# Kernel tuning notes

Hardware: AMD Instinct MI355X
Metric: run time of the kernel (lower is better)

## Reference

```python
import jax, jax.numpy as jnp
import numpy as np

N = 100000      # nodes (H3 lattice cells)
E = 600000      # directed edges (avg degree ~6, hexagonal)
D_IN, D_H, D_E = 256, 128, 64


def _init_linear(key, fan_in, fan_out):
    kw, kb = jax.random.split(key)
    s = 1.0 / np.sqrt(fan_in)
    W = jax.random.uniform(kw, (fan_in, fan_out), jnp.float32, -s, s)
    b = jax.random.uniform(kb, (fan_out,), jnp.float32, -s, s)
    return W, b


def setup_inputs() -> dict:
    key = jax.random.key(0)
    ks = jax.random.split(key, 8)
    W1, b1 = _init_linear(ks[2], D_IN, D_H)
    W2, b2 = _init_linear(ks[3], D_H, D_H)
    W3, b3 = _init_linear(ks[4], D_H, D_E)
    Wd1, bd1 = _init_linear(ks[5], D_E, D_H)
    Wd2, bd2 = _init_linear(ks[6], D_H, D_IN)
    return {
        "x": jax.random.normal(ks[0], (N, D_IN), jnp.float32),
        "edge_index": jax.random.randint(ks[1], (2, E), 0, N, dtype=jnp.int64),
        "W1": W1, "b1": b1, "W2": W2, "b2": b2, "W3": W3, "b3": b3,
        "Wd1": Wd1, "bd1": bd1, "Wd2": Wd2, "bd2": bd2,
    }


def _gcn_conv(x, src, dst, W, b):
    """PyG GCNConv: add self-loops, sym deg^{-1/2} norm, linear, scatter-add, bias."""
    n = x.shape[0]
    h = x @ W                                                  # [N, out]
    ones = jnp.ones(src.shape[0], x.dtype)
    deg = jax.ops.segment_sum(ones, dst, num_segments=n) + 1.0  # +1 for self-loop
    dinv = jax.lax.rsqrt(deg)                                   # deg >= 1 always
    coef = dinv[src] * dinv[dst]                                # [E]
    agg = jax.ops.segment_sum(h[src] * coef[:, None], dst, num_segments=n)
    agg = agg + h * (dinv * dinv)[:, None]                      # self-loop term
    return agg + b


def reference(x, edge_index, W1, b1, W2, b2, W3, b3, Wd1, bd1, Wd2, bd2):
    src, dst = edge_index[0], edge_index[1]
    # Encoder (dropout is identity in eval mode)
    h = jax.nn.relu(_gcn_conv(x, src, dst, W1, b1))
    h = jax.nn.relu(_gcn_conv(h, src, dst, W2, b2))
    z = _gcn_conv(h, src, dst, W3, b3)                          # [N, D_E]
    # Decoder
    x_hat = jax.nn.relu(z @ Wd1 + bd1) @ Wd2 + bd2              # [N, D_IN]
    return (z, x_hat)
```

## Files before the change

kernel.cpp:

```cpp
#include <hip/hip_runtime.h>

#define DIN 256
#define DH  128
#define DE  64

typedef __attribute__((ext_vector_type(8))) short short8;
typedef __attribute__((ext_vector_type(4))) float f32x4;
typedef __attribute__((ext_vector_type(4))) unsigned short us4;

__device__ inline unsigned short f2bf(float f) {
    unsigned u = __float_as_uint(f);
    return (unsigned short)((u + 0x7FFFu + ((u >> 16) & 1u)) >> 16);
}
__device__ inline float bf2f(unsigned short h) {
    return __uint_as_float((unsigned)h << 16);
}

__device__ inline void gload16(const void* g, void* l) {
    __builtin_amdgcn_global_load_lds(
        (const __attribute__((address_space(1))) void*)g,
        (__attribute__((address_space(3))) void*)l, 16, 0, 0);
}


__global__ void init_counts_kernel(int* __restrict__ counts, int n) {
    int i = blockIdx.x * blockDim.x + threadIdx.x;
    if (i < n) counts[i] = 0;
}

__global__ void count_edges_kernel(const int* __restrict__ dst,
                                   int* __restrict__ counts, int E) {
    int e = blockIdx.x * blockDim.x + threadIdx.x;
    if (e < E) atomicAdd(&counts[dst[e]], 1);
}

__global__ void dinv_kernel(const int* __restrict__ counts,
                            float* __restrict__ dinv, int n) {
    int i = blockIdx.x * blockDim.x + threadIdx.x;
    if (i < n) dinv[i] = rsqrtf((float)counts[i] + 1.0f);
}

__global__ void scan1_kernel(const int* __restrict__ counts,
                             int* __restrict__ rowptr,
                             int* __restrict__ blocksums, int n) {
    __shared__ int sd[256];
    int t = threadIdx.x;
    int base = blockIdx.x * 1024 + t * 4;
    int v[4];
#pragma unroll
    for (int i = 0; i < 4; i++) v[i] = (base + i < n) ? counts[base + i] : 0;
    int tsum = v[0] + v[1] + v[2] + v[3];
    sd[t] = tsum;
    __syncthreads();
    for (int off = 1; off < 256; off <<= 1) {
        int x = (t >= off) ? sd[t - off] : 0;
        __syncthreads();
        sd[t] += x;
        __syncthreads();
    }
    int p = sd[t] - tsum;
#pragma unroll
    for (int i = 0; i < 4; i++) {
        if (base + i < n) rowptr[base + i] = p;
        p += v[i];
    }
    if (t == 255) blocksums[blockIdx.x] = sd[255];
}

__global__ void scan2_kernel(int* __restrict__ blocksums, int nb) {
    if (threadIdx.x == 0 && blockIdx.x == 0) {
        int run = 0;
        for (int i = 0; i < nb; i++) {
            int x = blocksums[i];
            blocksums[i] = run;
            run += x;
        }
    }
}

__global__ void scan3_kernel(int* __restrict__ rowptr, int* __restrict__ cursor,
                             const int* __restrict__ blocksums, int n, int E) {
    int i = blockIdx.x * blockDim.x + threadIdx.x;
    if (i < n) {
        int r = rowptr[i] + blocksums[i >> 10];
        rowptr[i] = r;
        cursor[i] = r;
    }
    if (i == 0) rowptr[n] = E;
}

__global__ void fill_csr_kernel(const int* __restrict__ src,
                                const int* __restrict__ dst,
                                const float* __restrict__ dinv,
                                int* __restrict__ cursor,
                                int* __restrict__ csr_src,
                                float* __restrict__ csr_coef, int E) {
    int e = blockIdx.x * blockDim.x + threadIdx.x;
    if (e >= E) return;
    int s = src[e], d = dst[e];
    int pos = atomicAdd(&cursor[d], 1);
    csr_src[pos] = s;
    csr_coef[pos] = dinv[s] * dinv[d];
}


__global__ void wsplit_kernel(const float* __restrict__ W,
                              unsigned short* __restrict__ Wh,
                              unsigned short* __restrict__ Wl, int K, int N) {
    int i = blockIdx.x * blockDim.x + threadIdx.x;
    if (i >= K * N) return;
    int k = i / N, n = i % N;
    float v = W[i];
    unsigned short h = f2bf(v);
    Wh[(size_t)n * K + k] = h;
    Wl[(size_t)n * K + k] = f2bf(v - bf2f(h));
}


template <int K, int CF, bool AFP32, bool BIAS, bool RELU, bool SPLIT>
__global__ __launch_bounds__(256, 2) void mfma_gemm(
    const void* __restrict__ Agh, const void* __restrict__ Agl,
    const unsigned short* __restrict__ Wh,
    const unsigned short* __restrict__ Wl, const float* __restrict__ bias,
    float* __restrict__ C, unsigned short* __restrict__ Oh,
    unsigned short* __restrict__ Ol, int M, int NN) {
    __shared__ unsigned short Ath[128 * 64];
    __shared__ unsigned short Atl[128 * 64];

    int t = threadIdx.x;
    int wid = t >> 6;
    int l = t & 63;
    int lr = l & 15, lk = l >> 4;
    int row0 = blockIdx.x * 128;
    int col0 = blockIdx.y * (CF * 16);

    f32x4 acc0[CF], acc1[CF];
#pragma unroll
    for (int j = 0; j < CF; j++) {
        acc0[j] = (f32x4){0.f, 0.f, 0.f, 0.f};
        acc1[j] = (f32x4){0.f, 0.f, 0.f, 0.f};
    }

    for (int c = 0; c < K / 64; ++c) {
        int k0 = c * 64;
        if (AFP32) {
            const float* A = (const float*)Agh;
#pragma unroll
            for (int i = 0; i < 4; i++) {
                int row = i * 32 + (t >> 3);
                int gr = row0 + row;
                if (gr >= M) gr = M - 1;
                int ss = (t & 7) ^ (row & 7);
                const float* sp = A + (size_t)gr * K + k0 + ss * 8;
                float4 f0 = *(const float4*)sp;
                float4 f1 = *(const float4*)(sp + 4);
                float fv[8] = {f0.x, f0.y, f0.z, f0.w,
                               f1.x, f1.y, f1.z, f1.w};
                short8 hv, lv;
#pragma unroll
                for (int e = 0; e < 8; e++) {
                    unsigned short h = f2bf(fv[e]);
                    hv[e] = (short)h;
                    lv[e] = (short)f2bf(fv[e] - bf2f(h));
                }
                int li = (i * 256 + t) * 8;
                *(short8*)&Ath[li] = hv;
                *(short8*)&Atl[li] = lv;
            }
        } else {
            const unsigned short* Ah = (const unsigned short*)Agh;
            const unsigned short* Al = (const unsigned short*)Agl;
#pragma unroll
            for (int i = 0; i < 4; i++) {
                int row = i * 32 + (t >> 3);
                int gr = row0 + row;
                if (gr >= M) gr = M - 1;
                int ss = (t & 7) ^ (row & 7);
                size_t go = (size_t)gr * K + k0 + ss * 8;
                gload16(Ah + go, &Ath[(i * 256 + t) * 8]);
                gload16(Al + go, &Atl[(i * 256 + t) * 8]);
            }
        }
        __syncthreads();

#pragma unroll
        for (int ks = 0; ks < 2; ks++) {
            int r0 = wid * 32 + lr;
            int r1 = r0 + 16;
            int s = ks * 4 + lk;
            short8 a0h = *(const short8*)&Ath[r0 * 64 + (s ^ (r0 & 7)) * 8];
            short8 a0l = *(const short8*)&Atl[r0 * 64 + (s ^ (r0 & 7)) * 8];
            short8 a1h = *(const short8*)&Ath[r1 * 64 + (s ^ (r1 & 7)) * 8];
            short8 a1l = *(const short8*)&Atl[r1 * 64 + (s ^ (r1 & 7)) * 8];
            int kg = k0 + ks * 32 + lk * 8;
#pragma unroll
            for (int j = 0; j < CF; j++) {
                size_t wo = (size_t)(col0 + j * 16 + lr) * K + kg;
                short8 bh = *(const short8*)(Wh + wo);
                short8 bl = *(const short8*)(Wl + wo);
                acc0[j] = __builtin_amdgcn_mfma_f32_16x16x32_bf16(
                    a0h, bh, acc0[j], 0, 0, 0);
                acc0[j] = __builtin_amdgcn_mfma_f32_16x16x32_bf16(
                    a0l, bh, acc0[j], 0, 0, 0);
                acc0[j] = __builtin_amdgcn_mfma_f32_16x16x32_bf16(
                    a0h, bl, acc0[j], 0, 0, 0);
                acc1[j] = __builtin_amdgcn_mfma_f32_16x16x32_bf16(
                    a1h, bh, acc1[j], 0, 0, 0);
                acc1[j] = __builtin_amdgcn_mfma_f32_16x16x32_bf16(
                    a1l, bh, acc1[j], 0, 0, 0);
                acc1[j] = __builtin_amdgcn_mfma_f32_16x16x32_bf16(
                    a1h, bl, acc1[j], 0, 0, 0);
            }
        }
        __syncthreads();
    }

#pragma unroll
    for (int j = 0; j < CF; j++) {
        int col = col0 + j * 16 + lr;
        float bb = BIAS ? bias[col] : 0.f;
#pragma unroll
        for (int e = 0; e < 4; e++) {
            int r = row0 + wid * 32 + lk * 4 + e;
#pragma unroll
            for (int rf = 0; rf < 2; rf++) {
                int rr = r + rf * 16;
                if (rr >= M) continue;
                float v = (rf ? acc1[j][e] : acc0[j][e]) + bb;
                if (RELU) v = fmaxf(v, 0.f);
                if (SPLIT) {
                    unsigned short h = f2bf(v);
                    Oh[(size_t)rr * NN + col] = h;
                    Ol[(size_t)rr * NN + col] = f2bf(v - bf2f(h));
                } else {
                    C[(size_t)rr * NN + col] = v;
                }
            }
        }
    }
}


template <int D, bool RELU, bool WF32>
__global__ __launch_bounds__(256) void agg_kernel(
    const float* __restrict__ h, const float* __restrict__ dinv,
    const int* __restrict__ rowptr, const int* __restrict__ csr_src,
    const float* __restrict__ csr_coef, const float* __restrict__ bias,
    unsigned short* __restrict__ outh, unsigned short* __restrict__ outl,
    float* __restrict__ outf, int n) {
    constexpr int TPN = D / 16;
    constexpr int NPB = 256 / TPN;
    int v = blockIdx.x * NPB + threadIdx.x / TPN;
    int d = threadIdx.x % TPN;
    if (v >= n) return;

    float di = dinv[v];
    float s2 = di * di;
    const float* hv = h + (size_t)v * D + d * 4;
    float4 acc[4];
#pragma unroll
    for (int i = 0; i < 4; i++) {
        float4 sv = *(const float4*)(hv + i * TPN * 4);
        float4 bv = *(const float4*)&bias[(i * TPN + d) * 4];
        acc[i].x = fmaf(sv.x, s2, bv.x);
        acc[i].y = fmaf(sv.y, s2, bv.y);
        acc[i].z = fmaf(sv.z, s2, bv.z);
        acc[i].w = fmaf(sv.w, s2, bv.w);
    }

    int e0 = rowptr[v], e1 = rowptr[v + 1];
    int e = e0;
    for (; e + 2 <= e1; e += 2) {
        int s0 = csr_src[e], s1 = csr_src[e + 1];
        float c0 = csr_coef[e], c1 = csr_coef[e + 1];
        const float* p0 = h + (size_t)s0 * D + d * 4;
        const float* p1 = h + (size_t)s1 * D + d * 4;
        float4 g0[4], g1[4];
#pragma unroll
        for (int i = 0; i < 4; i++) g0[i] = *(const float4*)(p0 + i * TPN * 4);
#pragma unroll
        for (int i = 0; i < 4; i++) g1[i] = *(const float4*)(p1 + i * TPN * 4);
#pragma unroll
        for (int i = 0; i < 4; i++) {
            acc[i].x = fmaf(g0[i].x, c0, acc[i].x);
            acc[i].y = fmaf(g0[i].y, c0, acc[i].y);
            acc[i].z = fmaf(g0[i].z, c0, acc[i].z);
            acc[i].w = fmaf(g0[i].w, c0, acc[i].w);
            acc[i].x = fmaf(g1[i].x, c1, acc[i].x);
            acc[i].y = fmaf(g1[i].y, c1, acc[i].y);
            acc[i].z = fmaf(g1[i].z, c1, acc[i].z);
            acc[i].w = fmaf(g1[i].w, c1, acc[i].w);
        }
    }
    if (e < e1) {
        int s0 = csr_src[e];
        float c0 = csr_coef[e];
        const float* p0 = h + (size_t)s0 * D + d * 4;
#pragma unroll
        for (int i = 0; i < 4; i++) {
            float4 g = *(const float4*)(p0 + i * TPN * 4);
            acc[i].x = fmaf(g.x, c0, acc[i].x);
            acc[i].y = fmaf(g.y, c0, acc[i].y);
            acc[i].z = fmaf(g.z, c0, acc[i].z);
            acc[i].w = fmaf(g.w, c0, acc[i].w);
        }
    }

#pragma unroll
    for (int i = 0; i < 4; i++) {
        if (RELU) {
            acc[i].x = fmaxf(acc[i].x, 0.f);
            acc[i].y = fmaxf(acc[i].y, 0.f);
            acc[i].z = fmaxf(acc[i].z, 0.f);
            acc[i].w = fmaxf(acc[i].w, 0.f);
        }
        size_t o = (size_t)v * D + (i * TPN + d) * 4;
        float av[4] = {acc[i].x, acc[i].y, acc[i].z, acc[i].w};
        us4 hw, lw;
#pragma unroll
        for (int q = 0; q < 4; q++) {
            unsigned short hh = f2bf(av[q]);
            hw[q] = hh;
            lw[q] = f2bf(av[q] - bf2f(hh));
        }
        *(us4*)&outh[o] = hw;
        *(us4*)&outl[o] = lw;
        if (WF32) *(float4*)&outf[o] = acc[i];
    }
}


extern "C" void kernel_launch(void* const* d_in, const int* in_sizes, int n_in,
                              void* d_out, int out_size, void* d_ws,
                              size_t ws_size, hipStream_t stream) {
    const float* x   = (const float*)d_in[0];
    const int*   ei  = (const int*)d_in[1];
    const float* W1  = (const float*)d_in[2];
    const float* b1  = (const float*)d_in[3];
    const float* W2  = (const float*)d_in[4];
    const float* b2  = (const float*)d_in[5];
    const float* W3  = (const float*)d_in[6];
    const float* b3  = (const float*)d_in[7];
    const float* Wd1 = (const float*)d_in[8];
    const float* bd1 = (const float*)d_in[9];
    const float* Wd2 = (const float*)d_in[10];
    const float* bd2 = (const float*)d_in[11];

    const int N = in_sizes[0] / DIN;
    const int E = in_sizes[1] / 2;
    const int* src = ei;
    const int* dst = ei + E;

    char* w = (char*)d_ws;
    auto alloc = [&](size_t bytes) -> char* {
        char* p = w;
        w += (bytes + 255) & ~(size_t)255;
        return p;
    };
    int*   counts    = (int*)alloc((size_t)N * 4);
    float* dinv      = (float*)alloc((size_t)N * 4);
    int*   rowptr    = (int*)alloc((size_t)(N + 1) * 4);
    int*   cursor    = (int*)alloc((size_t)N * 4);
    int*   blocksums = (int*)alloc(4096);
    int*   csr_src   = (int*)alloc((size_t)E * 4);
    float* csr_coef  = (float*)alloc((size_t)E * 4);
    unsigned short* hh = (unsigned short*)alloc((size_t)N * DH * 2);
    unsigned short* hl = (unsigned short*)alloc((size_t)N * DH * 2);
    unsigned short* W1h  = (unsigned short*)alloc(DIN * DH * 2);
    unsigned short* W1l  = (unsigned short*)alloc(DIN * DH * 2);
    unsigned short* W2h  = (unsigned short*)alloc(DH * DH * 2);
    unsigned short* W2l  = (unsigned short*)alloc(DH * DH * 2);
    unsigned short* W3h  = (unsigned short*)alloc(DH * DE * 2);
    unsigned short* W3l  = (unsigned short*)alloc(DH * DE * 2);
    unsigned short* Wd1h = (unsigned short*)alloc(DE * DH * 2);
    unsigned short* Wd1l = (unsigned short*)alloc(DE * DH * 2);
    unsigned short* Wd2h = (unsigned short*)alloc(DH * DIN * 2);
    unsigned short* Wd2l = (unsigned short*)alloc(DH * DIN * 2);

    float* zout = (float*)d_out;
    float* xhat = zout + (size_t)N * DE;
    float* S1   = xhat;
    unsigned short* zh = (unsigned short*)(xhat + (size_t)N * DH);
    unsigned short* zl = zh + (size_t)N * DE;
    unsigned short* rh = hh;
    unsigned short* rl = hl;

    dim3 blk(256);
    int gN = (N + 255) / 256, gE = (E + 255) / 256;

    init_counts_kernel<<<gN, blk, 0, stream>>>(counts, N);
    count_edges_kernel<<<gE, blk, 0, stream>>>(dst, counts, E);
    dinv_kernel<<<gN, blk, 0, stream>>>(counts, dinv, N);
    int nb = (N + 1023) / 1024;
    scan1_kernel<<<nb, blk, 0, stream>>>(counts, rowptr, blocksums, N);
    scan2_kernel<<<1, 64, 0, stream>>>(blocksums, nb);
    scan3_kernel<<<gN, blk, 0, stream>>>(rowptr, cursor, blocksums, N, E);
    fill_csr_kernel<<<gE, blk, 0, stream>>>(src, dst, dinv, cursor, csr_src,
                                            csr_coef, E);

    wsplit_kernel<<<(DIN * DH + 255) / 256, blk, 0, stream>>>(W1, W1h, W1l,
                                                              DIN, DH);
    wsplit_kernel<<<(DH * DH + 255) / 256, blk, 0, stream>>>(W2, W2h, W2l,
                                                             DH, DH);
    wsplit_kernel<<<(DH * DE + 255) / 256, blk, 0, stream>>>(W3, W3h, W3l,
                                                             DH, DE);
    wsplit_kernel<<<(DE * DH + 255) / 256, blk, 0, stream>>>(Wd1, Wd1h, Wd1l,
                                                             DE, DH);
    wsplit_kernel<<<(DH * DIN + 255) / 256, blk, 0, stream>>>(Wd2, Wd2h, Wd2l,
                                                              DH, DIN);

    int gm = (N + 127) / 128;

    mfma_gemm<DIN, 8, true, false, false, false><<<dim3(gm, 1), blk, 0,
        stream>>>(x, nullptr, W1h, W1l, nullptr, S1, nullptr, nullptr, N, DH);
    agg_kernel<DH, true, false><<<(N + 31) / 32, blk, 0, stream>>>(
        S1, dinv, rowptr, csr_src, csr_coef, b1, hh, hl, nullptr, N);
    mfma_gemm<DH, 8, false, false, false, false><<<dim3(gm, 1), blk, 0,
        stream>>>(hh, hl, W2h, W2l, nullptr, S1, nullptr, nullptr, N, DH);
    agg_kernel<DH, true, false><<<(N + 31) / 32, blk, 0, stream>>>(
        S1, dinv, rowptr, csr_src, csr_coef, b2, hh, hl, nullptr, N);
    mfma_gemm<DH, 4, false, false, false, false><<<dim3(gm, 1), blk, 0,
        stream>>>(hh, hl, W3h, W3l, nullptr, S1, nullptr, nullptr, N, DE);
    agg_kernel<DE, false, true><<<(N + 63) / 64, blk, 0, stream>>>(
        S1, dinv, rowptr, csr_src, csr_coef, b3, zh, zl, zout, N);
    mfma_gemm<DE, 8, false, true, true, true><<<dim3(gm, 1), blk, 0,
        stream>>>(zh, zl, Wd1h, Wd1l, bd1, nullptr, rh, rl, N, DH);
    mfma_gemm<DH, 8, false, true, false, false><<<dim3(gm, 2), blk, 0,
        stream>>>(rh, rl, Wd2h, Wd2l, bd2, xhat, nullptr, nullptr, N, DIN);
}
```

Measured before the change: 736.8 us.

## Stage pre-tiled swizzled weight chunks in LDS for MFMA GEMMs

Weights are now split into bf16 hi/lo and written in a per-column-block, per-K-chunk tiled layout with an XOR swizzle. Each GEMM block copies its weight chunk into shared memory with async global-to-LDS loads alongside the A tile. The MFMA inner loop then reads B fragments from LDS instead of issuing global loads per fragment. This cuts repeated global/L2 traffic for weights, at the cost of extra LDS use, which may lower occupancy.

```diff
diff --git a/kernel.cpp b/kernel.cpp
--- a/kernel.cpp
+++ b/kernel.cpp
@@ -104,35 +104,46 @@
 }
 
 
-__global__ void wsplit_kernel(const float* __restrict__ W,
-                              unsigned short* __restrict__ Wh,
-                              unsigned short* __restrict__ Wl, int K, int N) {
+__global__ void wtile_kernel(const float* __restrict__ W,
+                             unsigned short* __restrict__ WtH,
+                             unsigned short* __restrict__ WtL, int K, int N,
+                             int CF16) {
     int i = blockIdx.x * blockDim.x + threadIdx.x;
     if (i >= K * N) return;
     int k = i / N, n = i % N;
     float v = W[i];
     unsigned short h = f2bf(v);
-    Wh[(size_t)n * K + k] = h;
-    Wl[(size_t)n * K + k] = f2bf(v - bf2f(h));
+    unsigned short lo = f2bf(v - bf2f(h));
+    int cb = n / CF16, cl = n % CF16;
+    int chunk = k >> 6, kk = k & 63;
+    int s = kk >> 3, e = kk & 7;
+    size_t idx = (size_t)(cb * (K >> 6) + chunk) * (CF16 * 64) + cl * 64 +
+                 ((s ^ (cl & 7)) * 8) + e;
+    WtH[idx] = h;
+    WtL[idx] = lo;
 }
 
 
 template <int K, int CF, bool AFP32, bool BIAS, bool RELU, bool SPLIT>
 __global__ __launch_bounds__(256, 2) void mfma_gemm(
     const void* __restrict__ Agh, const void* __restrict__ Agl,
-    const unsigned short* __restrict__ Wh,
-    const unsigned short* __restrict__ Wl, const float* __restrict__ bias,
+    const unsigned short* __restrict__ WtH,
+    const unsigned short* __restrict__ WtL, const float* __restrict__ bias,
     float* __restrict__ C, unsigned short* __restrict__ Oh,
     unsigned short* __restrict__ Ol, int M, int NN) {
+    constexpr int CF16 = CF * 16;
+    constexpr int CHUNKS = K / 64;
     __shared__ unsigned short Ath[128 * 64];
     __shared__ unsigned short Atl[128 * 64];
+    __shared__ unsigned short Bth[CF16 * 64];
+    __shared__ unsigned short Btl[CF16 * 64];
 
     int t = threadIdx.x;
     int wid = t >> 6;
     int l = t & 63;
     int lr = l & 15, lk = l >> 4;
     int row0 = blockIdx.x * 128;
-    int col0 = blockIdx.y * (CF * 16);
+    int col0 = blockIdx.y * CF16;
 
     f32x4 acc0[CF], acc1[CF];
 #pragma unroll
@@ -141,8 +152,15 @@
         acc1[j] = (f32x4){0.f, 0.f, 0.f, 0.f};
     }
 
-    for (int c = 0; c < K / 64; ++c) {
+    for (int c = 0; c < CHUNKS; ++c) {
         int k0 = c * 64;
+        size_t bbase = (size_t)(blockIdx.y * CHUNKS + c) * (CF16 * 64);
+#pragma unroll
+        for (int i = 0; i < CF16 / 32; i++) {
+            int idx = (i * 256 + t) * 8;
+            gload16(WtH + bbase + idx, &Bth[idx]);
+            gload16(WtL + bbase + idx, &Btl[idx]);
+        }
         if (AFP32) {
             const float* A = (const float*)Agh;
 #pragma unroll
@@ -192,12 +210,11 @@
             short8 a0l = *(const short8*)&Atl[r0 * 64 + (s ^ (r0 & 7)) * 8];
             short8 a1h = *(const short8*)&Ath[r1 * 64 + (s ^ (r1 & 7)) * 8];
             short8 a1l = *(const short8*)&Atl[r1 * 64 + (s ^ (r1 & 7)) * 8];
-            int kg = k0 + ks * 32 + lk * 8;
 #pragma unroll
             for (int j = 0; j < CF; j++) {
-                size_t wo = (size_t)(col0 + j * 16 + lr) * K + kg;
-                short8 bh = *(const short8*)(Wh + wo);
-                short8 bl = *(const short8*)(Wl + wo);
+                int bo = (j * 16 + lr) * 64 + ((s ^ (lr & 7)) * 8);
+                short8 bh = *(const short8*)&Bth[bo];
+                short8 bl = *(const short8*)&Btl[bo];
                 acc0[j] = __builtin_amdgcn_mfma_f32_16x16x32_bf16(
                     a0h, bh, acc0[j], 0, 0, 0);
                 acc0[j] = __builtin_amdgcn_mfma_f32_16x16x32_bf16(
@@ -398,16 +415,16 @@
     fill_csr_kernel<<<gE, blk, 0, stream>>>(src, dst, dinv, cursor, csr_src,
                                             csr_coef, E);
 
-    wsplit_kernel<<<(DIN * DH + 255) / 256, blk, 0, stream>>>(W1, W1h, W1l,
-                                                              DIN, DH);
-    wsplit_kernel<<<(DH * DH + 255) / 256, blk, 0, stream>>>(W2, W2h, W2l,
-                                                             DH, DH);
-    wsplit_kernel<<<(DH * DE + 255) / 256, blk, 0, stream>>>(W3, W3h, W3l,
-                                                             DH, DE);
-    wsplit_kernel<<<(DE * DH + 255) / 256, blk, 0, stream>>>(Wd1, Wd1h, Wd1l,
-                                                             DE, DH);
-    wsplit_kernel<<<(DH * DIN + 255) / 256, blk, 0, stream>>>(Wd2, Wd2h, Wd2l,
-                                                              DH, DIN);
+    wtile_kernel<<<(DIN * DH + 255) / 256, blk, 0, stream>>>(W1, W1h, W1l,
+                                                             DIN, DH, 128);
+    wtile_kernel<<<(DH * DH + 255) / 256, blk, 0, stream>>>(W2, W2h, W2l,
+                                                            DH, DH, 128);
+    wtile_kernel<<<(DH * DE + 255) / 256, blk, 0, stream>>>(W3, W3h, W3l,
+                                                            DH, DE, 64);
+    wtile_kernel<<<(DE * DH + 255) / 256, blk, 0, stream>>>(Wd1, Wd1h, Wd1l,
+                                                            DE, DH, 128);
+    wtile_kernel<<<(DH * DIN + 255) / 256, blk, 0, stream>>>(Wd2, Wd2h, Wd2l,
+                                                             DH, DIN, 128);
 
     int gm = (N + 127) / 128;
 
```

After: 600.5 us. 18.5% less time.
